# Performance work log

Measured on AMD Instinct MI355X. Metric: run time of the kernel, lower is better.

## Reference

```python
import jax, jax.numpy as jnp
import numpy as np

N = 10000   # num_nodes (= input feature dim, identity-style features)
E = 320000  # edges (avg degree 32)
P = 200000  # candidate node pairs
H1, H2 = 32, 16


def gcn_conv(x, W, b, edge_index, num_nodes):
    # PyG GCNConv: add self-loops, symmetric D^-1/2 (A+I) D^-1/2 normalization,
    # linear transform, scatter-add aggregation, then bias.
    loop = jnp.arange(num_nodes)
    src = jnp.concatenate([edge_index[0], loop])
    dst = jnp.concatenate([edge_index[1], loop])
    deg = jax.ops.segment_sum(jnp.ones_like(src, dtype=x.dtype), dst,
                              num_segments=num_nodes)  # includes self-loop, so deg >= 1
    dinv = jax.lax.rsqrt(deg)
    norm = dinv[src] * dinv[dst]                       # [E+N]
    h = x @ W                                          # [N, out]
    out = jax.ops.segment_sum(h[src] * norm[:, None], dst, num_segments=num_nodes)
    return out + b


def setup_inputs() -> dict:
    key = jax.random.key(0)
    ks = jax.random.split(key, 9)
    x = jax.random.normal(ks[0], (N, N), dtype=jnp.float32)
    edge_index = jax.random.randint(ks[1], (2, E), 0, N)
    pair_index = jax.random.randint(ks[2], (P, 2), 0, N)
    W1 = jax.random.normal(ks[3], (N, H1), dtype=jnp.float32) * 0.01
    b1 = jnp.zeros((H1,), jnp.float32)
    W2 = jax.random.normal(ks[4], (H1, H2), dtype=jnp.float32) * 0.1
    b2 = jnp.zeros((H2,), jnp.float32)
    Wfc = jax.random.normal(ks[5], (2 * H2, 1), dtype=jnp.float32) * 0.1
    bfc = jnp.zeros((1,), jnp.float32)
    return {"x": x, "edge_index": edge_index, "pair_index": pair_index,
            "W1": W1, "b1": b1, "W2": W2, "b2": b2, "Wfc": Wfc, "bfc": bfc}


def reference(x, edge_index, pair_index, W1, b1, W2, b2, Wfc, bfc):
    h = jax.nn.relu(gcn_conv(x, W1, b1, edge_index, N))   # [N, 32]
    h = gcn_conv(h, W2, b2, edge_index, N)                # [N, 16]
    pair = jnp.concatenate([h[pair_index[:, 0]], h[pair_index[:, 1]]], axis=1)  # [P, 32]
    return jax.nn.sigmoid(pair @ Wfc + bfc)               # [P, 1]
```

## Files before the change

### kernel.cpp

```cpp
#include <hip/hip_runtime.h>
#include <math.h>

#define NN 10000
#define EE 320000
#define PP 200000
#define NTILES 320

typedef _Float16 h8v __attribute__((ext_vector_type(8)));
typedef __attribute__((ext_vector_type(4))) float f4v;

#define GLOAD_LDS16(gsrc, ldst)                                                        \
    __builtin_amdgcn_global_load_lds((const __attribute__((address_space(1))) void*)(gsrc), \
                                     (__attribute__((address_space(3))) void*)(ldst), 16, 0, 0)

__device__ __forceinline__ ushort f2h(float f) {
    union { _Float16 h; ushort u; } c;
    c.h = (_Float16)f;
    return c.u;
}

__global__ void k_deg_count(const int* __restrict__ dst, int* __restrict__ degi) {
    int e = blockIdx.x * blockDim.x + threadIdx.x;
    if (e < EE) atomicAdd(&degi[dst[e]], 1);
}

__global__ void k_dinv(const int* __restrict__ degi, float* __restrict__ dinv) {
    int n = blockIdx.x * blockDim.x + threadIdx.x;
    if (n < NN) dinv[n] = rsqrtf((float)(degi[n] + 1));
}

__global__ void k_wprep(const float* __restrict__ W1, ushort* __restrict__ wf) {
    int t = blockIdx.x * blockDim.x + threadIdx.x;
    if (t >= NTILES * 2 * 64 * 8) return;
    int e = t & 7, lane = (t >> 3) & 63, ct = (t >> 9) & 1, g = t >> 10;
    int col = ct * 16 + (lane & 15);
    int k = g * 32 + (lane >> 4) * 8 + e;
    wf[t] = (k < NN) ? f2h(W1[(long)k * 32 + col]) : (ushort)0;
}

__global__ __launch_bounds__(256) void k_gemm1(const float* __restrict__ x,
                                               const ushort* __restrict__ w1f,
                                               const float* __restrict__ zp,
                                               float* __restrict__ h1_part) {
    __shared__ __align__(16) float  xs[4 * 3 * 2080];
    __shared__ __align__(16) ushort wlds[2560 * 8];
    const int tid = threadIdx.x;
    const int lane = tid & 63;
    const int w = tid >> 6;
    const int fl = lane & 15;
    const int khi = lane >> 4;
    const int ks = blockIdx.y;
    const int wrow0 = blockIdx.x * 64 + w * 16;
    const int k_begin = ks * 640;
    const long NN2 = (long)NN * NN;

    f4v acc0 = (f4v){0.f, 0.f, 0.f, 0.f};
    f4v acc1 = (f4v){0.f, 0.f, 0.f, 0.f};

#pragma unroll
    for (int i = 0; i < 10; ++i) {
        const int ul = i * 256 + w * 64 + lane;
        const ushort* srcw =
            w1f + (((long)(ks * 20 + (ul >> 7)) * 2 + ((ul >> 6) & 1)) * 64 + lane) * 8;
        GLOAD_LDS16(srcw, &wlds[(long)(i * 256 + w * 64) * 8]);
    }
    __syncthreads();

    const int sub = lane >> 5;
    const int kof = (lane & 31) * 4;
    auto stage = [&](int buf, int t) {
        const int k0 = k_begin + t * 128;
        float* dst = &xs[(w * 3 + buf) * 2080];
#pragma unroll
        for (int p = 0; p < 8; ++p) {
            long flat = (long)(wrow0 + p * 2 + sub) * NN + k0 + kof;
            const float* src = (flat + 4 <= NN2) ? (x + flat) : zp;
            GLOAD_LDS16(src, dst + p * 260);
        }
    };
    auto compute = [&](int buf, int t) {
        const float4* xrow =
            (const float4*)&xs[(w * 3 + buf) * 2080 + (fl >> 1) * 260 + (fl & 1) * 128];
#pragma unroll
        for (int kk = 0; kk < 4; ++kk) {
            const int gl = t * 4 + kk;
            h8v b0 = *(const h8v*)&wlds[((gl * 2 + 0) * 64 + lane) * 8];
            h8v b1 = *(const h8v*)&wlds[((gl * 2 + 1) * 64 + lane) * 8];
            float4 f0 = xrow[kk * 8 + khi * 2];
            float4 f1 = xrow[kk * 8 + khi * 2 + 1];
            union { h8v v; _Float16 h[8]; } a;
            a.h[0] = (_Float16)f0.x; a.h[1] = (_Float16)f0.y;
            a.h[2] = (_Float16)f0.z; a.h[3] = (_Float16)f0.w;
            a.h[4] = (_Float16)f1.x; a.h[5] = (_Float16)f1.y;
            a.h[6] = (_Float16)f1.z; a.h[7] = (_Float16)f1.w;
            acc0 = __builtin_amdgcn_mfma_f32_16x16x32_f16(a.v, b0, acc0, 0, 0, 0);
            acc1 = __builtin_amdgcn_mfma_f32_16x16x32_f16(a.v, b1, acc1, 0, 0, 0);
        }
    };

#define WAITV(n) asm volatile("s_waitcnt vmcnt(" #n ")" ::: "memory"); __builtin_amdgcn_sched_barrier(0)
#define WAITL()  asm volatile("s_waitcnt lgkmcnt(0)" ::: "memory");    __builtin_amdgcn_sched_barrier(0)

    stage(0, 0); stage(1, 1); stage(2, 2);
    WAITV(16); compute(0, 0); WAITL(); stage(0, 3);
    WAITV(16); compute(1, 1); WAITL(); stage(1, 4);
    WAITV(16); compute(2, 2);
    WAITV(8);  compute(0, 3);
    WAITV(0);  compute(1, 4);
#undef WAITV
#undef WAITL

    const long pbase = (long)ks * NN * 32;
#pragma unroll
    for (int ct = 0; ct < 2; ++ct) {
        f4v a = ct ? acc1 : acc0;
        const int col = ct * 16 + fl;
#pragma unroll
        for (int r = 0; r < 4; ++r) {
            int g = wrow0 + khi * 4 + r;
            if (g < NN) h1_part[pbase + (long)g * 32 + col] = a[r];
        }
    }
}

__global__ void k_selfinit1(const float* __restrict__ h1_part, const float* __restrict__ dinv,
                            float* __restrict__ h1_pre, float* __restrict__ out1) {
    int t = blockIdx.x * blockDim.x + threadIdx.x;
    if (t < NN * 32) {
        float sum = 0.f;
#pragma unroll
        for (int ks = 0; ks < 16; ++ks) sum += h1_part[(long)ks * NN * 32 + t];
        int n = t >> 5;
        float di = dinv[n];
        h1_pre[t] = sum;
        out1[t] = di * di * sum;
    }
}

__global__ void k_scatter1(const int* __restrict__ src, const int* __restrict__ dst,
                           const float* __restrict__ dinv, const float* __restrict__ h1_pre,
                           float* __restrict__ out1) {
    int t = blockIdx.x * blockDim.x + threadIdx.x;
    if (t >= EE * 32) return;
    int e = t >> 5, c = t & 31;
    int s = src[e], d = dst[e];
    float nrm = dinv[s] * dinv[d];
    atomicAdd(&out1[d * 32 + c], h1_pre[s * 32 + c] * nrm);
}

__global__ void k_bias_relu1(float* __restrict__ out1, const float* __restrict__ b1) {
    int t = blockIdx.x * blockDim.x + threadIdx.x;
    if (t < NN * 32) out1[t] = fmaxf(out1[t] + b1[t & 31], 0.f);
}

__global__ __launch_bounds__(256) void k_gemm2(const float* __restrict__ out1,
                                               const float* __restrict__ W2,
                                               float* __restrict__ h2_pre) {
    __shared__ float w2s[512];
    int tid = threadIdx.x;
    w2s[tid] = W2[tid & 511];
    if (tid < 256) w2s[256 + tid] = W2[256 + tid];
    __syncthreads();
    int c = tid & 15, yloc = tid >> 4;
    int n = blockIdx.x * 16 + yloc;
    if (n < NN) {
        float a = 0.f;
#pragma unroll
        for (int k = 0; k < 32; ++k) a += out1[n * 32 + k] * w2s[k * 16 + c];
        h2_pre[n * 16 + c] = a;
    }
}

__global__ void k_selfinit2(const float* __restrict__ h2_pre, const float* __restrict__ dinv,
                            float* __restrict__ out2) {
    int t = blockIdx.x * blockDim.x + threadIdx.x;
    if (t < NN * 16) {
        int n = t >> 4;
        float di = dinv[n];
        out2[t] = di * di * h2_pre[t];
    }
}

__global__ void k_scatter2(const int* __restrict__ src, const int* __restrict__ dst,
                           const float* __restrict__ dinv, const float* __restrict__ h2_pre,
                           float* __restrict__ out2) {
    int t = blockIdx.x * blockDim.x + threadIdx.x;
    if (t >= EE * 16) return;
    int e = t >> 4, c = t & 15;
    int s = src[e], d = dst[e];
    float nrm = dinv[s] * dinv[d];
    atomicAdd(&out2[d * 16 + c], h2_pre[s * 16 + c] * nrm);
}

__global__ void k_final2(const float* __restrict__ out2, const float* __restrict__ b2,
                         const float* __restrict__ Wfc, float* __restrict__ s_arr,
                         float* __restrict__ t_arr) {
    int n = blockIdx.x * blockDim.x + threadIdx.x;
    if (n >= NN) return;
    float s = 0.f, t = 0.f;
#pragma unroll
    for (int c = 0; c < 16; ++c) {
        float v = out2[n * 16 + c] + b2[c];
        s += v * Wfc[c];
        t += v * Wfc[16 + c];
    }
    s_arr[n] = s;
    t_arr[n] = t;
}

__global__ void k_pairs(const int* __restrict__ pair, const float* __restrict__ s_arr,
                        const float* __restrict__ t_arr, const float* __restrict__ bfc,
                        float* __restrict__ out) {
    int p = blockIdx.x * blockDim.x + threadIdx.x;
    if (p >= PP) return;
    const int2 ab = ((const int2*)pair)[p];
    float z = s_arr[ab.x] + t_arr[ab.y] + bfc[0];
    out[p] = 1.f / (1.f + expf(-z));
}

extern "C" void kernel_launch(void* const* d_in, const int* in_sizes, int n_in,
                              void* d_out, int out_size, void* d_ws, size_t ws_size,
                              hipStream_t stream) {
    const float* x    = (const float*)d_in[0];
    const int*   edge = (const int*)d_in[1];
    const int*   pair = (const int*)d_in[2];
    const float* W1   = (const float*)d_in[3];
    const float* b1   = (const float*)d_in[4];
    const float* W2   = (const float*)d_in[5];
    const float* b2   = (const float*)d_in[6];
    const float* Wfc  = (const float*)d_in[7];
    const float* bfc  = (const float*)d_in[8];
    float* out = (float*)d_out;
    float* ws  = (float*)d_ws;

    const int* src = edge;
    const int* dst = edge + EE;

    int*    degi    = (int*)ws;
    float*  dinv    = ws + NN;
    float*  h1_pre  = ws + 2 * NN;
    float*  out1    = ws + 34 * NN;
    float*  h2_pre  = ws + 66 * NN;
    float*  out2    = ws + 82 * NN;
    float*  s_arr   = ws + 98 * NN;
    float*  t_arr   = ws + 99 * NN;
    float*  zp      = ws + 100 * NN;
    ushort* w1f     = (ushort*)(ws + 100 * NN + 256);
    float*  h1_part = ws + 100 * NN + 256 + 163840;

    hipMemsetAsync(degi, 0, NN * sizeof(int), stream);
    hipMemsetAsync(zp, 0, 1024, stream);

    k_deg_count<<<(EE + 255) / 256, 256, 0, stream>>>(dst, degi);
    k_dinv<<<(NN + 255) / 256, 256, 0, stream>>>(degi, dinv);
    k_wprep<<<(NTILES * 2 * 64 * 8 + 255) / 256, 256, 0, stream>>>(W1, w1f);

    k_gemm1<<<dim3(157, 16), 256, 0, stream>>>(x, w1f, zp, h1_part);

    k_selfinit1<<<(NN * 32 + 255) / 256, 256, 0, stream>>>(h1_part, dinv, h1_pre, out1);
    k_scatter1<<<(EE * 32 + 255) / 256, 256, 0, stream>>>(src, dst, dinv, h1_pre, out1);
    k_bias_relu1<<<(NN * 32 + 255) / 256, 256, 0, stream>>>(out1, b1);

    k_gemm2<<<(NN + 15) / 16, 256, 0, stream>>>(out1, W2, h2_pre);

    k_selfinit2<<<(NN * 16 + 255) / 256, 256, 0, stream>>>(h2_pre, dinv, out2);
    k_scatter2<<<(EE * 16 + 255) / 256, 256, 0, stream>>>(src, dst, dinv, h2_pre, out2);

    k_final2<<<(NN + 255) / 256, 256, 0, stream>>>(out2, b2, Wfc, s_arr, t_arr);
    k_pairs<<<(PP + 255) / 256, 256, 0, stream>>>(pair, s_arr, t_arr, bfc, out);
}
```

Measured before the change: 208.7 us.

## Raise GEMM1 split-K count and drop software pipeline for single-shot tile loads

```diff
diff --git a/kernel.cpp b/kernel.cpp
--- a/kernel.cpp
+++ b/kernel.cpp
@@ -5,6 +5,8 @@
 #define EE 320000
 #define PP 200000
 #define NTILES 320
+#define KSPL 256
+#define NSPL 40
 
 typedef _Float16 h8v __attribute__((ext_vector_type(8)));
 typedef __attribute__((ext_vector_type(4))) float f4v;
@@ -42,8 +44,7 @@
                                                const ushort* __restrict__ w1f,
                                                const float* __restrict__ zp,
                                                float* __restrict__ h1_part) {
-    __shared__ __align__(16) float  xs[4 * 3 * 2080];
-    __shared__ __align__(16) ushort wlds[2560 * 8];
+    __shared__ __align__(16) float xs[4][16][260];
     const int tid = threadIdx.x;
     const int lane = tid & 63;
     const int w = tid >> 6;
@@ -51,64 +52,41 @@
     const int khi = lane >> 4;
     const int ks = blockIdx.y;
     const int wrow0 = blockIdx.x * 64 + w * 16;
-    const int k_begin = ks * 640;
+    const int kbase = ks * KSPL;
     const long NN2 = (long)NN * NN;
+
+#pragma unroll
+    for (int j = 0; j < 16; ++j) {
+        long flat = (long)(wrow0 + j) * NN + kbase + lane * 4;
+        const float* src = (flat + 4 <= NN2) ? (x + flat) : zp;
+        GLOAD_LDS16(src, &xs[w][j][0]);
+    }
+
+    h8v wr[8][2];
+#pragma unroll
+    for (int kk = 0; kk < 8; ++kk)
+#pragma unroll
+        for (int ct = 0; ct < 2; ++ct)
+            wr[kk][ct] = *(const h8v*)(w1f + ((long)((ks * 8 + kk) * 2 + ct) * 64 + lane) * 8);
+
+    asm volatile("s_waitcnt vmcnt(0)" ::: "memory");
+    __builtin_amdgcn_sched_barrier(0);
 
     f4v acc0 = (f4v){0.f, 0.f, 0.f, 0.f};
     f4v acc1 = (f4v){0.f, 0.f, 0.f, 0.f};
-
-#pragma unroll
-    for (int i = 0; i < 10; ++i) {
-        const int ul = i * 256 + w * 64 + lane;
-        const ushort* srcw =
-            w1f + (((long)(ks * 20 + (ul >> 7)) * 2 + ((ul >> 6) & 1)) * 64 + lane) * 8;
-        GLOAD_LDS16(srcw, &wlds[(long)(i * 256 + w * 64) * 8]);
-    }
-    __syncthreads();
-
-    const int sub = lane >> 5;
-    const int kof = (lane & 31) * 4;
-    auto stage = [&](int buf, int t) {
-        const int k0 = k_begin + t * 128;
-        float* dst = &xs[(w * 3 + buf) * 2080];
-#pragma unroll
-        for (int p = 0; p < 8; ++p) {
-            long flat = (long)(wrow0 + p * 2 + sub) * NN + k0 + kof;
-            const float* src = (flat + 4 <= NN2) ? (x + flat) : zp;
-            GLOAD_LDS16(src, dst + p * 260);
-        }
-    };
-    auto compute = [&](int buf, int t) {
-        const float4* xrow =
-            (const float4*)&xs[(w * 3 + buf) * 2080 + (fl >> 1) * 260 + (fl & 1) * 128];
-#pragma unroll
-        for (int kk = 0; kk < 4; ++kk) {
-            const int gl = t * 4 + kk;
-            h8v b0 = *(const h8v*)&wlds[((gl * 2 + 0) * 64 + lane) * 8];
-            h8v b1 = *(const h8v*)&wlds[((gl * 2 + 1) * 64 + lane) * 8];
-            float4 f0 = xrow[kk * 8 + khi * 2];
-            float4 f1 = xrow[kk * 8 + khi * 2 + 1];
-            union { h8v v; _Float16 h[8]; } a;
-            a.h[0] = (_Float16)f0.x; a.h[1] = (_Float16)f0.y;
-            a.h[2] = (_Float16)f0.z; a.h[3] = (_Float16)f0.w;
-            a.h[4] = (_Float16)f1.x; a.h[5] = (_Float16)f1.y;
-            a.h[6] = (_Float16)f1.z; a.h[7] = (_Float16)f1.w;
-            acc0 = __builtin_amdgcn_mfma_f32_16x16x32_f16(a.v, b0, acc0, 0, 0, 0);
-            acc1 = __builtin_amdgcn_mfma_f32_16x16x32_f16(a.v, b1, acc1, 0, 0, 0);
-        }
-    };
-
-#define WAITV(n) asm volatile("s_waitcnt vmcnt(" #n ")" ::: "memory"); __builtin_amdgcn_sched_barrier(0)
-#define WAITL()  asm volatile("s_waitcnt lgkmcnt(0)" ::: "memory");    __builtin_amdgcn_sched_barrier(0)
-
-    stage(0, 0); stage(1, 1); stage(2, 2);
-    WAITV(16); compute(0, 0); WAITL(); stage(0, 3);
-    WAITV(16); compute(1, 1); WAITL(); stage(1, 4);
-    WAITV(16); compute(2, 2);
-    WAITV(8);  compute(0, 3);
-    WAITV(0);  compute(1, 4);
-#undef WAITV
-#undef WAITL
+#pragma unroll
+    for (int kk = 0; kk < 8; ++kk) {
+        const float4* ap = (const float4*)&xs[w][fl][kk * 32 + khi * 8];
+        float4 f0 = ap[0];
+        float4 f1 = ap[1];
+        union { h8v v; _Float16 h[8]; } a;
+        a.h[0] = (_Float16)f0.x; a.h[1] = (_Float16)f0.y;
+        a.h[2] = (_Float16)f0.z; a.h[3] = (_Float16)f0.w;
+        a.h[4] = (_Float16)f1.x; a.h[5] = (_Float16)f1.y;
+        a.h[6] = (_Float16)f1.z; a.h[7] = (_Float16)f1.w;
+        acc0 = __builtin_amdgcn_mfma_f32_16x16x32_f16(a.v, wr[kk][0], acc0, 0, 0, 0);
+        acc1 = __builtin_amdgcn_mfma_f32_16x16x32_f16(a.v, wr[kk][1], acc1, 0, 0, 0);
+    }
 
     const long pbase = (long)ks * NN * 32;
 #pragma unroll
@@ -123,18 +101,20 @@
     }
 }
 
-__global__ void k_selfinit1(const float* __restrict__ h1_part, const float* __restrict__ dinv,
-                            float* __restrict__ h1_pre, float* __restrict__ out1) {
-    int t = blockIdx.x * blockDim.x + threadIdx.x;
-    if (t < NN * 32) {
-        float sum = 0.f;
-#pragma unroll
-        for (int ks = 0; ks < 16; ++ks) sum += h1_part[(long)ks * NN * 32 + t];
-        int n = t >> 5;
-        float di = dinv[n];
-        h1_pre[t] = sum;
-        out1[t] = di * di * sum;
-    }
+__global__ void k_selfinit1(const float4* __restrict__ h1_part4, const float* __restrict__ dinv,
+                            float4* __restrict__ h1_pre4, float4* __restrict__ out14) {
+    int t = blockIdx.x * blockDim.x + threadIdx.x;
+    if (t >= NN * 8) return;
+    float4 s = make_float4(0.f, 0.f, 0.f, 0.f);
+#pragma unroll
+    for (int ks = 0; ks < NSPL; ++ks) {
+        float4 v = h1_part4[(long)ks * NN * 8 + t];
+        s.x += v.x; s.y += v.y; s.z += v.z; s.w += v.w;
+    }
+    int n = t >> 3;
+    float d2 = dinv[n] * dinv[n];
+    h1_pre4[t] = s;
+    out14[t] = make_float4(s.x * d2, s.y * d2, s.z * d2, s.w * d2);
 }
 
 __global__ void k_scatter1(const int* __restrict__ src, const int* __restrict__ dst,
@@ -255,9 +235,10 @@
     k_dinv<<<(NN + 255) / 256, 256, 0, stream>>>(degi, dinv);
     k_wprep<<<(NTILES * 2 * 64 * 8 + 255) / 256, 256, 0, stream>>>(W1, w1f);
 
-    k_gemm1<<<dim3(157, 16), 256, 0, stream>>>(x, w1f, zp, h1_part);
-
-    k_selfinit1<<<(NN * 32 + 255) / 256, 256, 0, stream>>>(h1_part, dinv, h1_pre, out1);
+    k_gemm1<<<dim3(157, NSPL), 256, 0, stream>>>(x, w1f, zp, h1_part);
+
+    k_selfinit1<<<(NN * 8 + 255) / 256, 256, 0, stream>>>(
+        (const float4*)h1_part, dinv, (float4*)h1_pre, (float4*)out1);
     k_scatter1<<<(EE * 32 + 255) / 256, 256, 0, stream>>>(src, dst, dinv, h1_pre, out1);
     k_bias_relu1<<<(NN * 32 + 255) / 256, 256, 0, stream>>>(out1, b1);
 
```

Result: faster. 200.1 us (-4.1%).
